# Performance work log

Hardware: AMD Instinct MI355X
Metric: run time of the kernel (lower is better)

Reference implementation:

```python
import jax, jax.numpy as jnp
import numpy as np

V, D, T, B, H, L, FF = 32000, 1024, 1024, 2, 16, 2, 4096


def _ln(x, g, b, eps=1e-5):
    m = x.mean(-1, keepdims=True)
    v = ((x - m) ** 2).mean(-1, keepdims=True)
    return (x - m) * jax.lax.rsqrt(v + eps) * g + b


def setup_inputs() -> dict:
    key = jax.random.key(0)
    ks = jax.random.split(key, 16)
    s = 0.02  # init scale for stable softmax/logits
    return {
        "idx": jax.random.randint(ks[0], (B, T), 0, V),
        "targets": jax.random.randint(ks[1], (B, T), 0, V),
        "word_emb": jax.random.normal(ks[2], (V, D), jnp.float32) * s,
        "pos_emb": jax.random.normal(ks[3], (T, D), jnp.float32) * s,
        "ln1_g": jnp.ones((L, D), jnp.float32),
        "ln1_b": jnp.zeros((L, D), jnp.float32),
        "wq": jax.random.normal(ks[4], (L, D, D), jnp.float32) * s,
        "wk": jax.random.normal(ks[5], (L, D, D), jnp.float32) * s,
        "wv": jax.random.normal(ks[6], (L, D, D), jnp.float32) * s,
        "proj_w": jax.random.normal(ks[7], (L, D, D), jnp.float32) * s,
        "proj_b": jnp.zeros((L, D), jnp.float32),
        "ln2_g": jnp.ones((L, D), jnp.float32),
        "ln2_b": jnp.zeros((L, D), jnp.float32),
        "ff_w1": jax.random.normal(ks[8], (L, D, FF), jnp.float32) * s,
        "ff_b1": jnp.zeros((L, FF), jnp.float32),
        "ff_w2": jax.random.normal(ks[9], (L, FF, D), jnp.float32) * s,
        "ff_b2": jnp.zeros((L, D), jnp.float32),
        "lnf_g": jnp.ones((D,), jnp.float32),
        "lnf_b": jnp.zeros((D,), jnp.float32),
        "lm_w": jax.random.normal(ks[10], (D, V), jnp.float32) * s,
        "lm_b": jnp.zeros((V,), jnp.float32),
    }


def reference(word_emb, pos_emb, ln1_g, ln1_b, wq, wk, wv, proj_w, proj_b,
              ln2_g, ln2_b, ff_w1, ff_b1, ff_w2, ff_b2, lnf_g, lnf_b,
              lm_w, lm_b, idx, targets):
    b, t = idx.shape
    d = word_emb.shape[1]
    n_layer, n_head = wq.shape[0], H
    x = word_emb[idx] + pos_emb[:t]              # [B,T,D]
    causal = jnp.tril(jnp.ones((t, t), bool))
    maps = []
    for l in range(n_layer):
        h = _ln(x, ln1_g[l], ln1_b[l])
        q = (h @ wq[l]).reshape(b, t, n_head, -1)  # [B,T,H,hd]
        k = (h @ wk[l]).reshape(b, t, n_head, -1)
        v = (h @ wv[l]).reshape(b, t, n_head, -1)
        # NOTE: source scales by n_embd**-0.5 (full embedding dim), not head_size
        wei = jnp.einsum('bqhd,bkhd->bhqk', q, k) * (d ** -0.5)
        wei = jnp.where(causal, wei, -jnp.inf)
        wei = jax.nn.softmax(wei, axis=-1)        # [B,H,T,T]
        maps.append(wei)
        att = jnp.einsum('bhqk,bkhd->bqhd', wei, v).reshape(b, t, d)
        x = x + att @ proj_w[l] + proj_b[l]
        h2 = _ln(x, ln2_g[l], ln2_b[l])
        x = x + jax.nn.relu(h2 @ ff_w1[l] + ff_b1[l]) @ ff_w2[l] + ff_b2[l]
    x = _ln(x, lnf_g, lnf_b)
    logits = (x @ lm_w + lm_b).reshape(b * t, -1)  # [B*T, V]
    logp = jax.nn.log_softmax(logits, axis=-1)
    loss = -logp[jnp.arange(b * t), targets.reshape(-1)].mean()
    probs = jax.nn.log_softmax(x, axis=-1)         # source: LogSoftmax of final-LN x
    return (logits, loss, jnp.stack(maps), probs)
```

## Files before the change

### kernel.cpp

```cpp
#include <hip/hip_runtime.h>
#include <hip/hip_bf16.h>

#define VSZ 32000
#define DM  1024
#define TSEQ 1024
#define BB  2
#define HH  16
#define LL  2
#define FFD 4096
#define NTOK (BB*TSEQ)

static constexpr size_t LOGITS_OFF = 0;
static constexpr size_t LOSS_OFF   = (size_t)NTOK * VSZ;
static constexpr size_t MAPS_OFF   = LOSS_OFF + 1;
static constexpr size_t PROBS_OFF  = MAPS_OFF + (size_t)LL*BB*HH*TSEQ*TSEQ;

typedef __attribute__((ext_vector_type(8))) short bf8;
typedef __attribute__((ext_vector_type(4))) float f32x4;
typedef __attribute__((ext_vector_type(4))) short short4v;

__device__ __forceinline__ short f2bf(float f) {
  union { float f; unsigned u; } v; v.f = f;
  unsigned r = v.u + 0x7FFFu + ((v.u >> 16) & 1u);
  return (short)(r >> 16);
}

__device__ __forceinline__ float block_sum256(float v, float* sh) {
#pragma unroll
  for (int off = 32; off; off >>= 1) v += __shfl_down(v, off);
  int wid = threadIdx.x >> 6, lane = threadIdx.x & 63;
  if (lane == 0) sh[wid] = v;
  __syncthreads();
  v = sh[0] + sh[1] + sh[2] + sh[3];
  __syncthreads();
  return v;
}
__device__ __forceinline__ float block_max256(float v, float* sh) {
#pragma unroll
  for (int off = 32; off; off >>= 1) v = fmaxf(v, __shfl_down(v, off));
  int wid = threadIdx.x >> 6, lane = threadIdx.x & 63;
  if (lane == 0) sh[wid] = v;
  __syncthreads();
  v = fmaxf(fmaxf(sh[0], sh[1]), fmaxf(sh[2], sh[3]));
  __syncthreads();
  return v;
}

__global__ __launch_bounds__(256) void transpose_cvt(const float* __restrict__ W,
    short* __restrict__ Wt, int K, int N) {
  __shared__ float T[64][65];
  const int n0 = blockIdx.x * 64, k0 = blockIdx.y * 64;
  const int tid = threadIdx.x;
  const int lr = tid >> 4, lc4 = (tid & 15) * 4;
#pragma unroll
  for (int p = 0; p < 4; ++p) {
    int k = lr + p * 16;
    float4 w = *(const float4*)&W[(size_t)(k0 + k) * N + n0 + lc4];
    T[k][lc4] = w.x; T[k][lc4+1] = w.y; T[k][lc4+2] = w.z; T[k][lc4+3] = w.w;
  }
  __syncthreads();
#pragma unroll
  for (int p = 0; p < 4; ++p) {
    int n = lr + p * 16;
    short4v s;
    s.x = f2bf(T[lc4  ][n]);
    s.y = f2bf(T[lc4+1][n]);
    s.z = f2bf(T[lc4+2][n]);
    s.w = f2bf(T[lc4+3][n]);
    *(short4v*)&Wt[(size_t)(n0 + n) * K + k0 + lc4] = s;
  }
}

__global__ __launch_bounds__(256) void embed_kernel(const int* __restrict__ idx,
    const float* __restrict__ we, const float* __restrict__ pe, float* __restrict__ x) {
  int i = blockIdx.x * 256 + threadIdx.x;
  int n = i >> 10;
  int d = i & 1023;
  int t = n & (TSEQ - 1);
  x[i] = we[(size_t)idx[n] * DM + d] + pe[(size_t)t * DM + d];
}

template<int ALSO_F32>
__global__ __launch_bounds__(256) void ln_bf(const float* __restrict__ in,
    const float* __restrict__ g, const float* __restrict__ b,
    short* __restrict__ outb, float* __restrict__ outf) {
  __shared__ float sh[4];
  int row = blockIdx.x, tid = threadIdx.x;
  const float* xr = in + (size_t)row * DM;
  float4 v = *(const float4*)&xr[tid * 4];
  float s  = v.x + v.y + v.z + v.w;
  float s2 = v.x*v.x + v.y*v.y + v.z*v.z + v.w*v.w;
  s  = block_sum256(s, sh);
  s2 = block_sum256(s2, sh);
  float mean = s * (1.0f / DM);
  float var  = s2 * (1.0f / DM) - mean * mean;
  float inv  = rsqrtf(var + 1e-5f);
  float4 gv = *(const float4*)&g[tid * 4];
  float4 bv = *(const float4*)&b[tid * 4];
  float4 o;
  o.x = (v.x - mean) * inv * gv.x + bv.x;
  o.y = (v.y - mean) * inv * gv.y + bv.y;
  o.z = (v.z - mean) * inv * gv.z + bv.z;
  o.w = (v.w - mean) * inv * gv.w + bv.w;
  short4v ob;
  ob.x = f2bf(o.x); ob.y = f2bf(o.y); ob.z = f2bf(o.z); ob.w = f2bf(o.w);
  *(short4v*)&outb[(size_t)row * DM + tid * 4] = ob;
  if (ALSO_F32)
    *(float4*)&outf[(size_t)row * DM + tid * 4] = o;
}

template<int BIAS, int RES, int RELU, int OUTBF>
__global__ __launch_bounds__(256) void gemm_bb(const short* __restrict__ A, int lda,
    const short* __restrict__ Bt, const float* __restrict__ bias,
    void* __restrict__ Cv, int M, int K, int Nn) {
  __shared__ short As[128 * 40];
  __shared__ short Bs[128 * 40];
  float* Cf = (float*)Cv;
  short* Cb = (short*)Cv;
  const int tid  = threadIdx.x;
  const int bm   = blockIdx.x * 128, bn = blockIdx.y * 128;
  const int lane = tid & 63, wid = tid >> 6;
  const int wr = wid >> 1, wc = wid & 1;
  const int lr = lane & 15, lg = lane >> 4;
  const int sr = tid >> 1, sh = (tid & 1) * 16;

  f32x4 acc[4][4];
#pragma unroll
  for (int i = 0; i < 4; ++i)
#pragma unroll
    for (int j = 0; j < 4; ++j) acc[i][j] = (f32x4)0.f;

  for (int k0 = 0; k0 < K; k0 += 32) {
    const short* asrc = &A[(size_t)(bm + sr) * lda + k0 + sh];
    const short* bsrc = &Bt[(size_t)(bn + sr) * K + k0 + sh];
    *(bf8*)&As[sr * 40 + sh    ] = *(const bf8*)&asrc[0];
    *(bf8*)&As[sr * 40 + sh + 8] = *(const bf8*)&asrc[8];
    *(bf8*)&Bs[sr * 40 + sh    ] = *(const bf8*)&bsrc[0];
    *(bf8*)&Bs[sr * 40 + sh + 8] = *(const bf8*)&bsrc[8];
    __syncthreads();
    bf8 af[4], bfv[4];
#pragma unroll
    for (int i = 0; i < 4; ++i)
      af[i] = *(const bf8*)&As[(wr * 64 + i * 16 + lr) * 40 + lg * 8];
#pragma unroll
    for (int j = 0; j < 4; ++j)
      bfv[j] = *(const bf8*)&Bs[(wc * 64 + j * 16 + lr) * 40 + lg * 8];
#pragma unroll
    for (int i = 0; i < 4; ++i)
#pragma unroll
      for (int j = 0; j < 4; ++j)
        acc[i][j] = __builtin_amdgcn_mfma_f32_16x16x32_bf16(af[i], bfv[j], acc[i][j], 0, 0, 0);
    __syncthreads();
  }
#pragma unroll
  for (int i = 0; i < 4; ++i) {
#pragma unroll
    for (int v = 0; v < 4; ++v) {
      int row = bm + wr * 64 + i * 16 + lg * 4 + v;
      size_t rowb = (size_t)row * Nn;
#pragma unroll
      for (int j = 0; j < 4; ++j) {
        int col = bn + wc * 64 + j * 16 + lr;
        float val = acc[i][j][v];
        if (BIAS) val += bias[col];
        if (RES)  val += Cf[rowb + col];
        if (RELU) val = fmaxf(val, 0.f);
        if (OUTBF) Cb[rowb + col] = f2bf(val);
        else       Cf[rowb + col] = val;
      }
    }
  }
}

template<int BIAS>
__global__ __launch_bounds__(256) void gemm_lm_cvt(const float* __restrict__ A,
    const float* __restrict__ Bw, const float* __restrict__ bias,
    float* __restrict__ C, int M, int K, int Nn) {
  __shared__ short As[128 * 40];
  __shared__ short Bs[128 * 40];
  const int tid  = threadIdx.x;
  const int bm   = blockIdx.x * 128, bn = blockIdx.y * 128;
  const int lane = tid & 63, wid = tid >> 6;
  const int wr = wid >> 1, wc = wid & 1;
  const int lr = lane & 15, lg = lane >> 4;
  const int sar = tid >> 3, sak = (tid & 7) * 4;
  const int sbn = tid & 127, sbk = (tid >> 7) * 16;
  f32x4 acc[4][4];
#pragma unroll
  for (int i = 0; i < 4; ++i)
#pragma unroll
    for (int j = 0; j < 4; ++j) acc[i][j] = (f32x4)0.f;
  for (int k0 = 0; k0 < K; k0 += 32) {
#pragma unroll
    for (int p = 0; p < 4; ++p) {
      int row = sar + p * 32;
      float4 a4 = *(const float4*)&A[(size_t)(bm + row) * K + k0 + sak];
      short4v s4;
      s4.x = f2bf(a4.x); s4.y = f2bf(a4.y); s4.z = f2bf(a4.z); s4.w = f2bf(a4.w);
      *(short4v*)&As[row * 40 + sak] = s4;
    }
    {
      short tmp[16];
#pragma unroll
      for (int e = 0; e < 16; ++e)
        tmp[e] = f2bf(Bw[(size_t)(k0 + sbk + e) * Nn + bn + sbn]);
      *(bf8*)&Bs[sbn * 40 + sbk    ] = *(bf8*)&tmp[0];
      *(bf8*)&Bs[sbn * 40 + sbk + 8] = *(bf8*)&tmp[8];
    }
    __syncthreads();
    bf8 af[4], bfv[4];
#pragma unroll
    for (int i = 0; i < 4; ++i)
      af[i] = *(const bf8*)&As[(wr * 64 + i * 16 + lr) * 40 + lg * 8];
#pragma unroll
    for (int j = 0; j < 4; ++j)
      bfv[j] = *(const bf8*)&Bs[(wc * 64 + j * 16 + lr) * 40 + lg * 8];
#pragma unroll
    for (int i = 0; i < 4; ++i)
#pragma unroll
      for (int j = 0; j < 4; ++j)
        acc[i][j] = __builtin_amdgcn_mfma_f32_16x16x32_bf16(af[i], bfv[j], acc[i][j], 0, 0, 0);
    __syncthreads();
  }
#pragma unroll
  for (int i = 0; i < 4; ++i) {
#pragma unroll
    for (int v = 0; v < 4; ++v) {
      int row = bm + wr * 64 + i * 16 + lg * 4 + v;
      size_t rowb = (size_t)row * Nn;
#pragma unroll
      for (int j = 0; j < 4; ++j) {
        int col = bn + wc * 64 + j * 16 + lr;
        float val = acc[i][j][v];
        if (BIAS) val += bias[col];
        C[rowb + col] = val;
      }
    }
  }
}

__global__ __launch_bounds__(256) void attn_qkt(const float* __restrict__ qkv,
    float* __restrict__ maps_l) {
  __shared__ short Qs[64 * 72];
  __shared__ short Ks[64 * 72];
  const int tid = threadIdx.x;
  const int qi = blockIdx.x;
  const int bh = blockIdx.y;
  const int b = bh >> 4, h = bh & 15;
  const int q0 = qi * 64;
  const int lane = tid & 63, wid = tid >> 6;
  const int wr = wid >> 1, wc = wid & 1;
  const int lr = lane & 15, lg = lane >> 4;
  const int sr = tid >> 2, sc = (tid & 3) * 16;
  {
    const float* src = &qkv[(size_t)(b * TSEQ + q0 + sr) * 3072 + h * 64 + sc];
    short tmp[16];
#pragma unroll
    for (int e = 0; e < 16; ++e) tmp[e] = f2bf(src[e]);
    *(bf8*)&Qs[sr * 72 + sc    ] = *(bf8*)&tmp[0];
    *(bf8*)&Qs[sr * 72 + sc + 8] = *(bf8*)&tmp[8];
  }
  float* mbase = maps_l + (size_t)bh * TSEQ * TSEQ;
  for (int kt = 0; kt <= qi; ++kt) {
    const int k0 = kt * 64;
    {
      const float* src = &qkv[(size_t)(b * TSEQ + k0 + sr) * 3072 + 1024 + h * 64 + sc];
      short tmp[16];
#pragma unroll
      for (int e = 0; e < 16; ++e) tmp[e] = f2bf(src[e]);
      *(bf8*)&Ks[sr * 72 + sc    ] = *(bf8*)&tmp[0];
      *(bf8*)&Ks[sr * 72 + sc + 8] = *(bf8*)&tmp[8];
    }
    __syncthreads();
    f32x4 acc[2][2];
#pragma unroll
    for (int i = 0; i < 2; ++i)
#pragma unroll
      for (int j = 0; j < 2; ++j) acc[i][j] = (f32x4)0.f;
#pragma unroll
    for (int ds = 0; ds < 2; ++ds) {
      bf8 af[2], bfv[2];
#pragma unroll
      for (int i = 0; i < 2; ++i)
        af[i] = *(const bf8*)&Qs[(wr * 32 + i * 16 + lr) * 72 + ds * 32 + lg * 8];
#pragma unroll
      for (int j = 0; j < 2; ++j)
        bfv[j] = *(const bf8*)&Ks[(wc * 32 + j * 16 + lr) * 72 + ds * 32 + lg * 8];
#pragma unroll
      for (int i = 0; i < 2; ++i)
#pragma unroll
        for (int j = 0; j < 2; ++j)
          acc[i][j] = __builtin_amdgcn_mfma_f32_16x16x32_bf16(af[i], bfv[j], acc[i][j], 0, 0, 0);
    }
#pragma unroll
    for (int i = 0; i < 2; ++i)
#pragma unroll
      for (int v = 0; v < 4; ++v) {
        int row = q0 + wr * 32 + i * 16 + lg * 4 + v;
#pragma unroll
        for (int j = 0; j < 2; ++j) {
          int col = k0 + wc * 32 + j * 16 + lr;
          mbase[(size_t)row * TSEQ + col] = acc[i][j][v] * 0.03125f;
        }
      }
    __syncthreads();
  }
}

__global__ __launch_bounds__(256) void attn_softmax(float* __restrict__ maps_l) {
  __shared__ float sh[4];
  const int q = blockIdx.x, bh = blockIdx.y;
  const int tid = threadIdx.x;
  float* mrow = maps_l + (size_t)bh * TSEQ * TSEQ + (size_t)q * TSEQ;
  float s[4];
#pragma unroll
  for (int i = 0; i < 4; ++i) {
    int kp = tid + i * 256;
    s[i] = (kp <= q) ? mrow[kp] : -1e30f;
  }
  float m = block_max256(fmaxf(fmaxf(s[0], s[1]), fmaxf(s[2], s[3])), sh);
  float e[4]; float ssum = 0.f;
#pragma unroll
  for (int i = 0; i < 4; ++i) {
    int kp = tid + i * 256;
    e[i] = (kp <= q) ? __expf(s[i] - m) : 0.f;
    ssum += e[i];
  }
  ssum = block_sum256(ssum, sh);
  float inv = 1.f / ssum;
#pragma unroll
  for (int i = 0; i < 4; ++i) mrow[tid + i * 256] = e[i] * inv;
}

__global__ __launch_bounds__(256) void attn_av2(const float* __restrict__ maps_l,
    const float* __restrict__ qkv, short* __restrict__ att_bf) {
  __shared__ float Vs[64][68];
  __shared__ float Ws[32][66];
  const int tid = threadIdx.x;
  const int ql = tid >> 3, dg = tid & 7;
  const int q0 = blockIdx.x * 32;
  const int bh = blockIdx.y;
  const int b = bh >> 4, h = bh & 15;
  const float* wbase = maps_l + (size_t)bh * TSEQ * TSEQ;
  const int vr = tid >> 2, vc = (tid & 3) * 16;
  const int wrow = tid >> 3, wc8 = (tid & 7) * 8;
  float4 a0 = {0,0,0,0}, a1 = {0,0,0,0};
  const int ntiles = (q0 + 32 + 63) >> 6;
  for (int kt = 0; kt < ntiles; ++kt) {
    const int kb0 = kt * 64;
#pragma unroll
    for (int e = 0; e < 4; ++e)
      *(float4*)&Vs[vr][vc + e * 4] =
        *(const float4*)&qkv[(size_t)(b * TSEQ + kb0 + vr) * 3072 + 2048 + h * 64 + vc + e * 4];
#pragma unroll
    for (int e = 0; e < 4; ++e)
      *(float2*)&Ws[wrow][wc8 + e * 2] =
        *(const float2*)&wbase[(size_t)(q0 + wrow) * TSEQ + kb0 + wc8 + e * 2];
    __syncthreads();
#pragma unroll 8
    for (int k = 0; k < 64; ++k) {
      float w = Ws[ql][k];
      float4 v0 = *(const float4*)&Vs[k][dg * 8];
      float4 v1 = *(const float4*)&Vs[k][dg * 8 + 4];
      a0.x += w * v0.x; a0.y += w * v0.y; a0.z += w * v0.z; a0.w += w * v0.w;
      a1.x += w * v1.x; a1.y += w * v1.y; a1.z += w * v1.z; a1.w += w * v1.w;
    }
    __syncthreads();
  }
  short* orow = &att_bf[(size_t)(b * TSEQ + q0 + ql) * DM + h * 64 + dg * 8];
  short4v s0, s1;
  s0.x = f2bf(a0.x); s0.y = f2bf(a0.y); s0.z = f2bf(a0.z); s0.w = f2bf(a0.w);
  s1.x = f2bf(a1.x); s1.y = f2bf(a1.y); s1.z = f2bf(a1.z); s1.w = f2bf(a1.w);
  *(short4v*)&orow[0] = s0;
  *(short4v*)&orow[4] = s1;
}

__global__ __launch_bounds__(256) void loss_rows(const float* __restrict__ logits,
    const int* __restrict__ targets, float* __restrict__ rowloss) {
  __shared__ float sh[4];
  int row = blockIdx.x, tid = threadIdx.x;
  const float* lr = logits + (size_t)row * VSZ;
  float m = -1e30f;
  for (int i = tid; i < VSZ; i += 256) m = fmaxf(m, lr[i]);
  m = block_max256(m, sh);
  float ssum = 0.f;
  for (int i = tid; i < VSZ; i += 256) ssum += __expf(lr[i] - m);
  ssum = block_sum256(ssum, sh);
  if (tid == 0)
    rowloss[row] = m + logf(ssum) - lr[targets[row]];
}
__global__ __launch_bounds__(256) void loss_reduce(const float* __restrict__ rowloss,
    float* __restrict__ out) {
  __shared__ float sh[4];
  float s = 0.f;
  for (int i = threadIdx.x; i < NTOK; i += 256) s += rowloss[i];
  s = block_sum256(s, sh);
  if (threadIdx.x == 0) out[0] = s * (1.0f / NTOK);
}
__global__ __launch_bounds__(256) void probs_rows(const float* __restrict__ xf,
    float* __restrict__ out) {
  __shared__ float sh[4];
  int row = blockIdx.x, tid = threadIdx.x;
  const float* xr = xf + (size_t)row * DM;
  float4 v = *(const float4*)&xr[tid * 4];
  float m = block_max256(fmaxf(fmaxf(v.x, v.y), fmaxf(v.z, v.w)), sh);
  float ssum = __expf(v.x-m) + __expf(v.y-m) + __expf(v.z-m) + __expf(v.w-m);
  ssum = block_sum256(ssum, sh);
  float lg = m + logf(ssum);
  float* orow = out + (size_t)row * DM + tid * 4;
  orow[0] = v.x - lg;
  orow[1] = v.y - lg;
  orow[2] = v.z - lg;
  orow[3] = v.w - lg;
}

extern "C" void kernel_launch(void* const* d_in, const int* in_sizes, int n_in,
                              void* d_out, int out_size, void* d_ws, size_t ws_size,
                              hipStream_t stream) {
  const int*   idx      = (const int*)  d_in[0];
  const int*   targets  = (const int*)  d_in[1];
  const float* word_emb = (const float*)d_in[2];
  const float* pos_emb  = (const float*)d_in[3];
  const float* ln1_g    = (const float*)d_in[4];
  const float* ln1_b    = (const float*)d_in[5];
  const float* wq       = (const float*)d_in[6];
  const float* wk       = (const float*)d_in[7];
  const float* wv       = (const float*)d_in[8];
  const float* proj_w   = (const float*)d_in[9];
  const float* proj_b   = (const float*)d_in[10];
  const float* ln2_g    = (const float*)d_in[11];
  const float* ln2_b    = (const float*)d_in[12];
  const float* ff_w1    = (const float*)d_in[13];
  const float* ff_b1    = (const float*)d_in[14];
  const float* ff_w2    = (const float*)d_in[15];
  const float* ff_b2    = (const float*)d_in[16];
  const float* lnf_g    = (const float*)d_in[17];
  const float* lnf_b    = (const float*)d_in[18];
  const float* lm_w     = (const float*)d_in[19];
  const float* lm_b     = (const float*)d_in[20];

  float* outf   = (float*)d_out;
  float* logits = outf + LOGITS_OFF;
  float* lossp  = outf + LOSS_OFF;
  float* maps   = outf + MAPS_OFF;
  float* probs  = outf + PROBS_OFF;

  const size_t ND = (size_t)NTOK * DM;
  float* x    = (float*)d_ws;
  float* xf   = x + ND;
  float* qkvb = xf + ND;
  float* rowloss = qkvb + (size_t)NTOK * 3072;
  short* h_bf   = (short*)(rowloss + NTOK);
  short* att_bf = h_bf + ND;
  short* ffh_bf = att_bf + ND;
  short* xf_bf  = ffh_bf + (size_t)NTOK * FFD;
  char*  ws_end = (char*)(xf_bf + ND);
  const size_t act_bytes = (size_t)(ws_end - (char*)d_ws);
  const size_t lmwt_bytes = (size_t)VSZ * DM * sizeof(short);
  const int lm_fast = (ws_size >= act_bytes + lmwt_bytes);
  short* lm_wt = (short*)ws_end;

  const size_t PLW = (size_t)3 * DM * DM + DM * DM + (size_t)DM * FFD + (size_t)FFD * DM;
  short* wt_base = (short*)logits;
  auto layer_wt = [&](int l) { return wt_base + (size_t)l * PLW; };

  dim3 b256(256);
  for (int l = 0; l < LL; ++l) {
    short* qkvt = layer_wt(l);
    short* projt = qkvt + (size_t)3 * DM * DM;
    short* ff1t  = projt + (size_t)DM * DM;
    short* ff2t  = ff1t + (size_t)DM * FFD;
    const size_t wo = (size_t)l * DM * DM;
    transpose_cvt<<<dim3(16, 16), b256, 0, stream>>>(wq + wo, qkvt,                 DM, DM);
    transpose_cvt<<<dim3(16, 16), b256, 0, stream>>>(wk + wo, qkvt + (size_t)DM*DM, DM, DM);
    transpose_cvt<<<dim3(16, 16), b256, 0, stream>>>(wv + wo, qkvt + (size_t)2*DM*DM, DM, DM);
    transpose_cvt<<<dim3(16, 16), b256, 0, stream>>>(proj_w + wo, projt, DM, DM);
    transpose_cvt<<<dim3(FFD/64, 16), b256, 0, stream>>>(ff_w1 + (size_t)l*DM*FFD, ff1t, DM, FFD);
    transpose_cvt<<<dim3(16, FFD/64), b256, 0, stream>>>(ff_w2 + (size_t)l*FFD*DM, ff2t, FFD, DM);
  }
  if (lm_fast)
    transpose_cvt<<<dim3(VSZ/64, 16), b256, 0, stream>>>(lm_w, lm_wt, DM, VSZ);

  embed_kernel<<<dim3((NTOK * DM) / 256), b256, 0, stream>>>(idx, word_emb, pos_emb, x);

  for (int l = 0; l < LL; ++l) {
    short* qkvt = layer_wt(l);
    short* projt = qkvt + (size_t)3 * DM * DM;
    short* ff1t  = projt + (size_t)DM * DM;
    short* ff2t  = ff1t + (size_t)DM * FFD;
    ln_bf<0><<<dim3(NTOK), b256, 0, stream>>>(x, ln1_g + l * DM, ln1_b + l * DM, h_bf, nullptr);
    gemm_bb<0,0,0,0><<<dim3(NTOK/128, 3072/128), b256, 0, stream>>>(h_bf, DM, qkvt, nullptr, qkvb, NTOK, DM, 3072);
    float* maps_l = maps + (size_t)l * BB * HH * TSEQ * TSEQ;
    attn_qkt<<<dim3(TSEQ/64, BB*HH), b256, 0, stream>>>(qkvb, maps_l);
    attn_softmax<<<dim3(TSEQ, BB*HH), b256, 0, stream>>>(maps_l);
    attn_av2<<<dim3(TSEQ/32, BB*HH), b256, 0, stream>>>(maps_l, qkvb, att_bf);
    gemm_bb<1,1,0,0><<<dim3(NTOK/128, DM/128), b256, 0, stream>>>(att_bf, DM, projt, proj_b + l * DM, x, NTOK, DM, DM);
    ln_bf<0><<<dim3(NTOK), b256, 0, stream>>>(x, ln2_g + l * DM, ln2_b + l * DM, h_bf, nullptr);
    gemm_bb<1,0,1,1><<<dim3(NTOK/128, FFD/128), b256, 0, stream>>>(h_bf, DM, ff1t, ff_b1 + l * FFD, ffh_bf, NTOK, DM, FFD);
    gemm_bb<1,1,0,0><<<dim3(NTOK/128, DM/128), b256, 0, stream>>>(ffh_bf, FFD, ff2t, ff_b2 + l * DM, x, NTOK, FFD, DM);
  }

  ln_bf<1><<<dim3(NTOK), b256, 0, stream>>>(x, lnf_g, lnf_b, xf_bf, xf);
  if (lm_fast)
    gemm_bb<1,0,0,0><<<dim3(NTOK/128, VSZ/128), b256, 0, stream>>>(xf_bf, DM, lm_wt, lm_b, logits, NTOK, DM, VSZ);
  else
    gemm_lm_cvt<1><<<dim3(NTOK/128, VSZ/128), b256, 0, stream>>>(xf, lm_w, lm_b, logits, NTOK, DM, VSZ);
  loss_rows<<<dim3(NTOK), b256, 0, stream>>>(logits, targets, rowloss);
  loss_reduce<<<dim3(1), b256, 0, stream>>>(rowloss, lossp);
  probs_rows<<<dim3(NTOK), b256, 0, stream>>>(xf, probs);

  (void)in_sizes; (void)n_in; (void)out_size;
}
```

Baseline: 1.298 ms.

## Use direct global-to-LDS loads in GEMM and merge weight transposes into one launch

The GEMM tile loads now use global_load_lds so data goes straight from global memory into LDS without a register round trip. The LDS row pitch drops from 40 to 32 shorts to fit the contiguous layout that instruction requires, which may bring back bank conflicts on the fragment reads. Separately, the twelve per-layer weight transpose/convert launches are folded into a single transpose_all kernel to cut launch overhead.

```diff
diff --git a/kernel.cpp b/kernel.cpp
--- a/kernel.cpp
+++ b/kernel.cpp
@@ -25,6 +25,12 @@
   return (short)(r >> 16);
 }
 
+__device__ __forceinline__ void gload16(const void* g, void* l) {
+  __builtin_amdgcn_global_load_lds(
+      (const __attribute__((address_space(1))) void*)g,
+      (__attribute__((address_space(3))) void*)l, 16, 0, 0);
+}
+
 __device__ __forceinline__ float block_sum256(float v, float* sh) {
 #pragma unroll
   for (int off = 32; off; off >>= 1) v += __shfl_down(v, off);
@@ -44,6 +50,52 @@
   v = fmaxf(fmaxf(sh[0], sh[1]), fmaxf(sh[2], sh[3]));
   __syncthreads();
   return v;
+}
+
+static constexpr size_t PLW = (size_t)4 * DM * DM + (size_t)DM * FFD + (size_t)FFD * DM;
+__global__ __launch_bounds__(256) void transpose_all(const float* __restrict__ wq,
+    const float* __restrict__ wk, const float* __restrict__ wv,
+    const float* __restrict__ proj_w, const float* __restrict__ ff_w1,
+    const float* __restrict__ ff_w2, short* __restrict__ wt_base) {
+  __shared__ float T[64][65];
+  const int bid = blockIdx.x;
+  const int l = bid / 3072, r = bid % 3072;
+  short* qbase = wt_base + (size_t)l * PLW;
+  const float* W; short* Wt; int K, N, tn, tk;
+  if (r < 1024) {
+    int s = r >> 8, rr = r & 255;
+    W = (s == 0 ? wq : (s == 1 ? wk : (s == 2 ? wv : proj_w))) + (size_t)l * DM * DM;
+    Wt = qbase + (size_t)s * DM * DM;
+    K = DM; N = DM; tn = rr & 15; tk = rr >> 4;
+  } else if (r < 2048) {
+    int rr = r - 1024;
+    W = ff_w1 + (size_t)l * DM * FFD; Wt = qbase + (size_t)4 * DM * DM;
+    K = DM; N = FFD; tn = rr & 63; tk = rr >> 6;
+  } else {
+    int rr = r - 2048;
+    W = ff_w2 + (size_t)l * FFD * DM; Wt = qbase + (size_t)4 * DM * DM + (size_t)DM * FFD;
+    K = FFD; N = DM; tn = rr & 15; tk = rr >> 4;
+  }
+  const int n0 = tn * 64, k0 = tk * 64;
+  const int tid = threadIdx.x;
+  const int lr = tid >> 4, lc4 = (tid & 15) * 4;
+#pragma unroll
+  for (int p = 0; p < 4; ++p) {
+    int k = lr + p * 16;
+    float4 w = *(const float4*)&W[(size_t)(k0 + k) * N + n0 + lc4];
+    T[k][lc4] = w.x; T[k][lc4+1] = w.y; T[k][lc4+2] = w.z; T[k][lc4+3] = w.w;
+  }
+  __syncthreads();
+#pragma unroll
+  for (int p = 0; p < 4; ++p) {
+    int n = lr + p * 16;
+    short4v s;
+    s.x = f2bf(T[lc4  ][n]);
+    s.y = f2bf(T[lc4+1][n]);
+    s.z = f2bf(T[lc4+2][n]);
+    s.w = f2bf(T[lc4+3][n]);
+    *(short4v*)&Wt[(size_t)(n0 + n) * K + k0 + lc4] = s;
+  }
 }
 
 __global__ __launch_bounds__(256) void transpose_cvt(const float* __restrict__ W,
@@ -113,8 +165,8 @@
 __global__ __launch_bounds__(256) void gemm_bb(const short* __restrict__ A, int lda,
     const short* __restrict__ Bt, const float* __restrict__ bias,
     void* __restrict__ Cv, int M, int K, int Nn) {
-  __shared__ short As[128 * 40];
-  __shared__ short Bs[128 * 40];
+  __shared__ short As[128 * 32];
+  __shared__ short Bs[128 * 32];
   float* Cf = (float*)Cv;
   short* Cb = (short*)Cv;
   const int tid  = threadIdx.x;
@@ -122,7 +174,8 @@
   const int lane = tid & 63, wid = tid >> 6;
   const int wr = wid >> 1, wc = wid & 1;
   const int lr = lane & 15, lg = lane >> 4;
-  const int sr = tid >> 1, sh = (tid & 1) * 16;
+  const int srow = lane >> 2;
+  const int schunk = (lane & 3) * 8;
 
   f32x4 acc[4][4];
 #pragma unroll
@@ -131,20 +184,21 @@
     for (int j = 0; j < 4; ++j) acc[i][j] = (f32x4)0.f;
 
   for (int k0 = 0; k0 < K; k0 += 32) {
-    const short* asrc = &A[(size_t)(bm + sr) * lda + k0 + sh];
-    const short* bsrc = &Bt[(size_t)(bn + sr) * K + k0 + sh];
-    *(bf8*)&As[sr * 40 + sh    ] = *(const bf8*)&asrc[0];
-    *(bf8*)&As[sr * 40 + sh + 8] = *(const bf8*)&asrc[8];
-    *(bf8*)&Bs[sr * 40 + sh    ] = *(const bf8*)&bsrc[0];
-    *(bf8*)&Bs[sr * 40 + sh + 8] = *(const bf8*)&bsrc[8];
+#pragma unroll
+    for (int t = 0; t < 2; ++t) {
+      const int issue = wid * 2 + t;
+      const int row = issue * 16 + srow;
+      gload16(&A[(size_t)(bm + row) * lda + k0 + schunk], &As[issue * 512]);
+      gload16(&Bt[(size_t)(bn + row) * K  + k0 + schunk], &Bs[issue * 512]);
+    }
     __syncthreads();
     bf8 af[4], bfv[4];
 #pragma unroll
     for (int i = 0; i < 4; ++i)
-      af[i] = *(const bf8*)&As[(wr * 64 + i * 16 + lr) * 40 + lg * 8];
+      af[i] = *(const bf8*)&As[(wr * 64 + i * 16 + lr) * 32 + lg * 8];
 #pragma unroll
     for (int j = 0; j < 4; ++j)
-      bfv[j] = *(const bf8*)&Bs[(wc * 64 + j * 16 + lr) * 40 + lg * 8];
+      bfv[j] = *(const bf8*)&Bs[(wc * 64 + j * 16 + lr) * 32 + lg * 8];
 #pragma unroll
     for (int i = 0; i < 4; ++i)
 #pragma unroll
@@ -460,24 +514,11 @@
   const int lm_fast = (ws_size >= act_bytes + lmwt_bytes);
   short* lm_wt = (short*)ws_end;
 
-  const size_t PLW = (size_t)3 * DM * DM + DM * DM + (size_t)DM * FFD + (size_t)FFD * DM;
   short* wt_base = (short*)logits;
   auto layer_wt = [&](int l) { return wt_base + (size_t)l * PLW; };
 
   dim3 b256(256);
-  for (int l = 0; l < LL; ++l) {
-    short* qkvt = layer_wt(l);
-    short* projt = qkvt + (size_t)3 * DM * DM;
-    short* ff1t  = projt + (size_t)DM * DM;
-    short* ff2t  = ff1t + (size_t)DM * FFD;
-    const size_t wo = (size_t)l * DM * DM;
-    transpose_cvt<<<dim3(16, 16), b256, 0, stream>>>(wq + wo, qkvt,                 DM, DM);
-    transpose_cvt<<<dim3(16, 16), b256, 0, stream>>>(wk + wo, qkvt + (size_t)DM*DM, DM, DM);
-    transpose_cvt<<<dim3(16, 16), b256, 0, stream>>>(wv + wo, qkvt + (size_t)2*DM*DM, DM, DM);
-    transpose_cvt<<<dim3(16, 16), b256, 0, stream>>>(proj_w + wo, projt, DM, DM);
-    transpose_cvt<<<dim3(FFD/64, 16), b256, 0, stream>>>(ff_w1 + (size_t)l*DM*FFD, ff1t, DM, FFD);
-    transpose_cvt<<<dim3(16, FFD/64), b256, 0, stream>>>(ff_w2 + (size_t)l*FFD*DM, ff2t, FFD, DM);
-  }
+  transpose_all<<<dim3(2 * 3072), b256, 0, stream>>>(wq, wk, wv, proj_w, ff_w1, ff_w2, wt_base);
   if (lm_fast)
     transpose_cvt<<<dim3(VSZ/64, 16), b256, 0, stream>>>(lm_w, lm_wt, DM, VSZ);
 
```

New measurement: 1.220 ms. -6.0%, faster.
